# Kernel optimization log

Measured on AMD Instinct MI355X. Metric: run time of the kernel, lower is better.

## Reference

```python
import jax, jax.numpy as jnp
import numpy as np

B, F, Q, E = 256, 128, 4096, 128
TAU = 0.2
P_DROP = 0.5
NUM_SAMPLES = 128  # hardcoded in forward: compute_scores(..., num_samples=128)
NUM_POS = 1
EASY_UB = 0.5
HARD_LB = 0.5


def setup_inputs() -> dict:
    k = jax.random.key(0)
    ks = jax.random.split(k, 8)
    query = jax.random.normal(ks[0], (B, F), jnp.float32)
    key = jax.random.normal(ks[1], (B, F), jnp.float32)
    teacher = jax.random.normal(ks[2], (B, F), jnp.float32)
    negatives = jax.random.normal(ks[3], (F, Q), jnp.float32)
    # random_maskout masks: rand <= p -> zero out
    mask_t = jax.random.uniform(ks[4], (E, B, F)) <= P_DROP
    mask_n = jax.random.uniform(ks[5], (E, F, Q)) <= P_DROP
    # compute_scores sampling mask: rand <= num_samples/Q
    score_mask = jax.random.uniform(ks[6], (E, B, Q)) <= (NUM_SAMPLES / Q)
    # bootstrap over batch dim: for each (e,q) column, sample B row indices with replacement
    idx = jax.random.randint(ks[7], (E, Q, B), 0, B)
    boot = jnp.zeros((E, Q, B), bool).at[
        jnp.arange(E)[:, None, None], jnp.arange(Q)[None, :, None], idx
    ].set(True)
    boot_mask = jnp.transpose(boot, (0, 2, 1))  # (E,B,Q)
    return dict(query=query, key=key, teacher=teacher, negatives=negatives,
                mask_t=mask_t, mask_n=mask_n, score_mask=score_mask, boot_mask=boot_mask)


def _masked_softmax(x, mask, axis):
    # matches torch masked_fill(~mask, -inf) + softmax; masked entries -> 0 prob
    z = jnp.where(mask, x, -jnp.inf)
    m = jnp.max(z, axis=axis, keepdims=True)
    m = jnp.where(jnp.isfinite(m), m, 0.0)  # guard fully-masked slices
    e = jnp.where(mask, jnp.exp(z - m), 0.0)
    return e / jnp.maximum(e.sum(axis=axis, keepdims=True), 1e-30)


def _l2norm(x, axis):
    n = jnp.sqrt(jnp.sum(x * x, axis=axis, keepdims=True))
    return x / jnp.maximum(n, 1e-12)


def reference(query, key, teacher, negatives, mask_t, mask_n, score_mask, boot_mask):
    negatives = jax.lax.stop_gradient(negatives)  # negatives.detach().clone()
    logits_pos = jnp.sum(query * key, axis=1, keepdims=True)      # (B,1)
    logits_neg = query @ negatives                                 # (B,Q)
    logits = jnp.concatenate([logits_pos, logits_neg], axis=1) / TAU
    moco_loss = -jax.nn.log_softmax(logits, axis=1)[:, 0].mean()   # CE with target 0

    # ---- teacher similarities (torch.no_grad) ----
    t = _l2norm(jnp.where(mask_t, 0.0, teacher[None, :, :]), 2)    # (E,B,F)
    n = _l2norm(jnp.where(mask_n, 0.0, negatives[None, :, :]), 1)  # (E,F,Q)
    sim = jax.lax.stop_gradient(jnp.einsum('ebf,efq->ebq', t, n) / TAU)

    # ---- scores: masked softmax over Q, masked mean over E ----
    probs = _masked_softmax(sim, score_mask, axis=2)               # (E,B,Q)
    cnt_e = jnp.maximum(score_mask.sum(axis=0).astype(sim.dtype), 1.0)
    scores = probs.sum(axis=0) / cnt_e                             # (B,Q)

    # ---- uncertainty: masked entropy over batch dim ----
    p = _masked_softmax(sim, boot_mask, axis=1) + 1e-7             # (E,B,Q)
    ent = -(p * jnp.log(p))
    cnt_b = jnp.maximum(boot_mask.sum(axis=1).astype(sim.dtype), 1.0)  # (E,Q)
    uncertainty = (ent.sum(axis=1) / cnt_b).mean(axis=0, keepdims=True)  # (1,Q)

    log_sm_neg = jax.nn.log_softmax(logits[:, 1:], axis=1)         # (B,Q)

    def _pos_loss(pos_mask_row):
        pm = jnp.broadcast_to(pos_mask_row, (B, Q))
        s = jnp.where(pm, scores, -jnp.inf)
        _, idx = jax.lax.top_k(s, NUM_POS)                         # (B,k)
        loss = -jnp.take_along_axis(log_sm_neg, idx, axis=1).mean(axis=1).mean()
        mask = jnp.zeros((B, Q), bool).at[jnp.arange(B)[:, None], idx].set(True)
        return loss, mask

    ub = jnp.quantile(uncertainty, EASY_UB, axis=1)                # (1,)
    easy_loss, easy_mask = _pos_loss(uncertainty <= ub)
    lb = jnp.quantile(uncertainty, HARD_LB, axis=1)
    hard_loss, hard_mask = _pos_loss(uncertainty >= lb)

    return moco_loss, logits, easy_loss, easy_mask, hard_loss, hard_mask
```

## Files before the change

kernel.cpp:

```cpp
#include <hip/hip_runtime.h>
#include <cmath>

typedef unsigned char u8;
typedef unsigned short u16;
typedef unsigned int u32;
typedef __attribute__((ext_vector_type(8))) short s8v;
typedef __attribute__((ext_vector_type(4))) float f32x4;

#define B 256
#define F 128
#define Q 4096
#define E 128
#define QW 128
#define INV_TAU 5.0f
#define CAP 256

#define W_SCORES 0u
#define W_CNT    1048576u
#define W_UNC    2097152u
#define W_CNTB   2101248u
#define W_NLSE   2134016u
#define W_MOCO   2134272u
#define W_EASY   2134528u
#define W_HARD   2134784u
#define W_UB     2135040u
#define W_INVN   2135296u
#define W_AF     2659584u
#define W_PB     4756736u
#define W_PS     8951040u
#define W_PN     13145344u
#define W_ENT    15242496u
#define NZERO    2134016u

#define O_MOCO   0u
#define O_LOGITS 1u
#define O_ELOSS  1048833u
#define O_EMASK  1048834u
#define O_HLOSS  2097410u
#define O_HMASK  2097411u

static __device__ __forceinline__ u16 f2bf(float x) {
    unsigned int u = __builtin_bit_cast(unsigned int, x);
    unsigned int r = (u + 0x7FFFu + ((u >> 16) & 1u)) >> 16;
    return (u16)r;
}

__global__ void k_zero(float4* __restrict__ p) {
    p[(size_t)blockIdx.x * 256 + threadIdx.x] = make_float4(0.f, 0.f, 0.f, 0.f);
}

__global__ void __launch_bounds__(256) k_pack(const u8* __restrict__ boot,
                                              const u8* __restrict__ smask,
                                              const u8* __restrict__ maskn,
                                              u32* __restrict__ pb, u32* __restrict__ ps,
                                              u32* __restrict__ pn) {
    int z = blockIdx.z;
    int Rin = (z == 2) ? F : B;
    if (z == 2 && blockIdx.x >= 2048) return;
    const u8* in = (z == 0) ? boot : (z == 1) ? smask : maskn;
    u32* out = (z == 0) ? pb : (z == 1) ? ps : pn;
    __shared__ u32 lds[64 * 133];
    int t = threadIdx.x;
    int r0 = blockIdx.x * 64;
    int q0 = blockIdx.y * 512;
    int qw0 = q0 >> 5;
    #pragma unroll
    for (int i = 0; i < 8; i++) {
        int w = i * 256 + t;
        int row = w >> 5, c = w & 31;
        uint4 v = *(const uint4*)&in[(size_t)(r0 + row) * Q + q0 + c * 16];
        int base = row * 133 + c * 4;
        lds[base] = v.x; lds[base + 1] = v.y; lds[base + 2] = v.z; lds[base + 3] = v.w;
    }
    __syncthreads();
    int e = r0 / Rin, rr = r0 % Rin;
    #pragma unroll
    for (int k = 0; k < 4; k++) {
        int qw = (t >> 6) + k * 4;
        int r = t & 63;
        u32 w = 0;
        #pragma unroll
        for (int j = 0; j < 8; j++) {
            u32 u = lds[r * 133 + qw * 8 + j];
            w |= ((u & 1u) | ((u >> 7) & 2u) | ((u >> 14) & 4u) | ((u >> 21) & 8u)) << (j * 4);
        }
        out[((size_t)e * QW + qw0 + qw) * Rin + rr + r] = w;
    }
}

__global__ void k_afrag(const float* __restrict__ teacher, const u8* __restrict__ mask_t,
                        u16* __restrict__ af) {
    int eb = blockIdx.x;
    int e  = eb >> 8;
    int b  = eb & (B - 1);
    int f  = threadIdx.x;
    float v = mask_t[(size_t)eb * F + f] ? 0.f : teacher[b * F + f];
    float ss = v * v;
    #pragma unroll
    for (int o = 32; o > 0; o >>= 1) ss += __shfl_down(ss, o);
    __shared__ float s2[2];
    if ((threadIdx.x & 63) == 0) s2[threadIdx.x >> 6] = ss;
    __syncthreads();
    float d = fmaxf(sqrtf(s2[0] + s2[1]), 1e-12f);
    float t = v / d;
    int bg = b >> 4, m = b & 15;
    int kb = f >> 5, quad = (f >> 3) & 3, j = f & 7;
    int lane = quad * 16 + m;
    af[((((size_t)e * 16 + bg) * 4 + kb) * 64 + lane) * 8 + j] = f2bf(t);
}

__global__ void __launch_bounds__(256) k_invn(const float* __restrict__ neg,
                                              const u32* __restrict__ pn,
                                              float* __restrict__ invn) {
    __shared__ u32 lds[32 * 128];
    int e = blockIdx.x, t = threadIdx.x;
    int qblk = blockIdx.y;
    size_t base = ((size_t)e * QW + qblk * 32) * F;
    #pragma unroll
    for (int k = 0; k < 16; k++) lds[t + 256 * k] = pn[base + t + 256 * k];
    __syncthreads();
    int q0 = qblk * 1024 + t * 4;
    int qwl = (t * 4) >> 5;
    int sh = (t * 4) & 31;
    float s0 = 0.f, s1 = 0.f, s2 = 0.f, s3 = 0.f;
    #pragma unroll 4
    for (int f = 0; f < F; f++) {
        float4 v = *(const float4*)&neg[(size_t)f * Q + q0];
        u32 w = lds[qwl * 128 + f] >> sh;
        if (!(w & 1u)) s0 = fmaf(v.x, v.x, s0);
        if (!(w & 2u)) s1 = fmaf(v.y, v.y, s1);
        if (!(w & 4u)) s2 = fmaf(v.z, v.z, s2);
        if (!(w & 8u)) s3 = fmaf(v.w, v.w, s3);
    }
    float4 r;
    r.x = INV_TAU / fmaxf(sqrtf(s0), 1e-12f);
    r.y = INV_TAU / fmaxf(sqrtf(s1), 1e-12f);
    r.z = INV_TAU / fmaxf(sqrtf(s2), 1e-12f);
    r.w = INV_TAU / fmaxf(sqrtf(s3), 1e-12f);
    *(float4*)&invn[(size_t)e * Q + q0] = r;
}

__global__ void __launch_bounds__(256) k_fused(
        const u16* __restrict__ af, const float* __restrict__ neg,
        const u32* __restrict__ pn, const float* __restrict__ invn,
        const u32* __restrict__ pb, const u32* __restrict__ ps,
        float* __restrict__ unc, uint2* __restrict__ ent_buf,
        int* __restrict__ cnt_buf, int e0) {
    __shared__ u16 bfrag[4][4][512];
    __shared__ u32 bw[2][256], sw[2][256];
    __shared__ u32 pnl[2][128];
    __shared__ float invl[64];
    __shared__ float sstat[4][64], cstat[4][64], estat[4][64];
    __shared__ float carr[64];
    __shared__ int sbase[256];

    int qb = blockIdx.x;
    int el = blockIdx.y, e = e0 + el;
    int t = threadIdx.x;
    int q0 = qb * 64;
    int qw0 = qb * 2;

    bw[0][t] = pb[((size_t)e * QW + qw0) * B + t];
    bw[1][t] = pb[((size_t)e * QW + qw0 + 1) * B + t];
    sw[0][t] = ps[((size_t)e * QW + qw0) * B + t];
    sw[1][t] = ps[((size_t)e * QW + qw0 + 1) * B + t];
    if (t < 128) {
        pnl[0][t] = pn[((size_t)e * QW + qw0) * F + t];
        pnl[1][t] = pn[((size_t)e * QW + qw0 + 1) * F + t];
    } else if (t < 192) {
        invl[t - 128] = invn[(size_t)e * Q + q0 + (t - 128)];
    }
    __syncthreads();

    #pragma unroll
    for (int s = 0; s < 4; s++) {
        int slot = t + 256 * s;
        int qg = slot >> 8;
        int r = slot & 255;
        int kb = r >> 6, lane2 = r & 63;
        int ql = qg * 16 + (lane2 & 15);
        int fb = kb * 32 + (lane2 >> 4) * 8;
        float iv = invl[ql];
        const u32* pw = pnl[ql >> 5];
        int sh = ql & 31;
        u16 tmp[8];
        #pragma unroll
        for (int j = 0; j < 8; j++) {
            u32 bit = (pw[fb + j] >> sh) & 1u;
            float v = bit ? 0.f : neg[(size_t)(fb + j) * Q + q0 + ql] * iv;
            tmp[j] = f2bf(v);
        }
        *(s8v*)&bfrag[qg][kb][lane2 * 8] = *(const s8v*)tmp;
    }
    __syncthreads();

    int wave = t >> 6, lane = t & 63;
    int colb = lane & 15, quad = lane >> 4;
    f32x4 acc[4][4];
    #pragma unroll
    for (int bgi = 0; bgi < 4; bgi++) {
        int bg = wave * 4 + bgi;
        s8v a[4];
        #pragma unroll
        for (int kb = 0; kb < 4; kb++)
            a[kb] = *(const s8v*)&af[((((size_t)e * 16 + bg) * 4 + kb) * 64 + lane) * 8];
        #pragma unroll
        for (int qg = 0; qg < 4; qg++) {
            f32x4 c4 = {0.f, 0.f, 0.f, 0.f};
            #pragma unroll
            for (int kb = 0; kb < 4; kb++) {
                s8v bv = *(const s8v*)&bfrag[qg][kb][lane * 8];
                c4 = __builtin_amdgcn_mfma_f32_16x16x32_bf16(a[kb], bv, c4, 0, 0, 0);
            }
            acc[bgi][qg] = c4;
        }
    }

    #pragma unroll
    for (int bgi = 0; bgi < 4; bgi++)
        #pragma unroll
        for (int qg = 0; qg < 4; qg++)
            #pragma unroll
            for (int r = 0; r < 4; r++)
                acc[bgi][qg][r] = __expf(acc[bgi][qg][r]);

    float sloc[4] = {0.f, 0.f, 0.f, 0.f}, cloc[4] = {0.f, 0.f, 0.f, 0.f};
    #pragma unroll
    for (int bgi = 0; bgi < 4; bgi++) {
        int b0 = (wave * 4 + bgi) * 16 + quad * 4;
        uint4 w0 = *(const uint4*)&bw[0][b0];
        uint4 w1 = *(const uint4*)&bw[1][b0];
        u32 W0[4] = {w0.x, w0.y, w0.z, w0.w};
        u32 W1[4] = {w1.x, w1.y, w1.z, w1.w};
        #pragma unroll
        for (int r = 0; r < 4; r++)
            #pragma unroll
            for (int qg = 0; qg < 4; qg++) {
                u32 w = (qg & 2) ? W1[r] : W0[r];
                int bpos = (qg & 1) * 16 + colb;
                if ((w >> bpos) & 1u) {
                    sloc[qg] += acc[bgi][qg][r];
                    cloc[qg] += 1.f;
                }
            }
    }
    #pragma unroll
    for (int qg = 0; qg < 4; qg++) {
        sloc[qg] += __shfl_xor(sloc[qg], 16); sloc[qg] += __shfl_xor(sloc[qg], 32);
        cloc[qg] += __shfl_xor(cloc[qg], 16); cloc[qg] += __shfl_xor(cloc[qg], 32);
    }
    if (quad == 0)
        #pragma unroll
        for (int qg = 0; qg < 4; qg++) {
            sstat[wave][qg * 16 + colb] = sloc[qg];
            cstat[wave][qg * 16 + colb] = cloc[qg];
        }
    __syncthreads();
    float invS[4];
    #pragma unroll
    for (int qg = 0; qg < 4; qg++) {
        int c = qg * 16 + colb;
        float S = sstat[0][c] + sstat[1][c] + sstat[2][c] + sstat[3][c];
        invS[qg] = 1.f / fmaxf(S, 1e-30f);
    }
    if (wave == 0 && quad == 0)
        #pragma unroll
        for (int qg = 0; qg < 4; qg++) {
            int c = qg * 16 + colb;
            carr[c] = cstat[0][c] + cstat[1][c] + cstat[2][c] + cstat[3][c];
        }

    const float P0 = 1e-7f;
    const float C0 = 1.61180954e-6f;
    float eloc[4] = {0.f, 0.f, 0.f, 0.f};
    #pragma unroll
    for (int bgi = 0; bgi < 4; bgi++) {
        int b0 = (wave * 4 + bgi) * 16 + quad * 4;
        uint4 w0 = *(const uint4*)&bw[0][b0];
        uint4 w1 = *(const uint4*)&bw[1][b0];
        u32 W0[4] = {w0.x, w0.y, w0.z, w0.w};
        u32 W1[4] = {w1.x, w1.y, w1.z, w1.w};
        #pragma unroll
        for (int r = 0; r < 4; r++)
            #pragma unroll
            for (int qg = 0; qg < 4; qg++) {
                u32 w = (qg & 2) ? W1[r] : W0[r];
                int bpos = (qg & 1) * 16 + colb;
                if ((w >> bpos) & 1u) {
                    float p = acc[bgi][qg][r] * invS[qg] + P0;
                    eloc[qg] -= p * __logf(p);
                } else {
                    eloc[qg] += C0;
                }
            }
    }
    #pragma unroll
    for (int qg = 0; qg < 4; qg++) {
        eloc[qg] += __shfl_xor(eloc[qg], 16); eloc[qg] += __shfl_xor(eloc[qg], 32);
    }
    if (quad == 0)
        #pragma unroll
        for (int qg = 0; qg < 4; qg++) estat[wave][qg * 16 + colb] = eloc[qg];

    {
        u32 a0 = sw[0][t], a1 = sw[1][t];
        int n = __popc(a0) + __popc(a1);
        int base = 0;
        if (n) base = atomicAdd(&cnt_buf[el * B + t], n);
        sbase[t] = base;
    }
    __syncthreads();

    if (t < 64) {
        float tot = estat[0][t] + estat[1][t] + estat[2][t] + estat[3][t];
        atomicAdd(&unc[q0 + t], tot / fmaxf(carr[t], 1.f));
    }

    u32 cmask = 0x00010001u << colb;
    #pragma unroll
    for (int bgi = 0; bgi < 4; bgi++) {
        int b0 = (wave * 4 + bgi) * 16 + quad * 4;
        uint4 s0 = *(const uint4*)&sw[0][b0];
        uint4 s1 = *(const uint4*)&sw[1][b0];
        u32 S0[4] = {s0.x, s0.y, s0.z, s0.w};
        u32 S1[4] = {s1.x, s1.y, s1.z, s1.w};
        #pragma unroll
        for (int r = 0; r < 4; r++) {
            if (!((S0[r] | S1[r]) & cmask)) continue;
            int bs = sbase[b0 + r];
            int p0 = __popc(S0[r]);
            #pragma unroll
            for (int qg = 0; qg < 4; qg++) {
                int bpos = (qg & 1) * 16 + colb;
                u32 w = (qg & 2) ? S1[r] : S0[r];
                if ((w >> bpos) & 1u) {
                    int rank = __popc(w & ((1u << bpos) - 1u)) + ((qg & 2) ? p0 : 0);
                    int pos = bs + rank;
                    if (pos < CAP) {
                        uint2 en;
                        en.x = (unsigned)(q0 + qg * 16 + colb);
                        en.y = __builtin_bit_cast(unsigned, acc[bgi][qg][r]);
                        ent_buf[((size_t)(el * B + b0 + r)) * CAP + pos] = en;
                    }
                }
            }
        }
    }
}

__global__ void __launch_bounds__(512) k_scores(
        const uint2* __restrict__ ent_buf, const int* __restrict__ cnt_buf,
        float* __restrict__ sacc, float* __restrict__ cacc, int ecnt) {
    __shared__ float srow[Q];
    __shared__ float crow[Q];
    __shared__ int cl[E];
    int b = blockIdx.x, t = threadIdx.x;
    #pragma unroll
    for (int j = 0; j < 8; j++) { srow[t + 512 * j] = 0.f; crow[t + 512 * j] = 0.f; }
    if (t < ecnt) {
        int c = cnt_buf[t * B + b];
        cl[t] = (c > CAP) ? CAP : c;
    }
    __syncthreads();
    int wave = t >> 6, lane = t & 63;
    for (int el = wave; el < ecnt; el += 8) {
        int c = cl[el];
        if (c == 0) continue;
        const uint2* p = ent_buf + (size_t)(el * B + b) * CAP;
        uint2 ev[4]; int ne = 0;
        float s = 0.f;
        for (int i = lane; i < c; i += 64) {
            ev[ne] = p[i];
            s += __builtin_bit_cast(float, ev[ne].y);
            ne++;
        }
        #pragma unroll
        for (int off = 32; off > 0; off >>= 1) s += __shfl_xor(s, off);
        float iS = 1.f / fmaxf(s, 1e-30f);
        for (int k = 0; k < ne; k++) {
            atomicAdd(&srow[ev[k].x], __builtin_bit_cast(float, ev[k].y) * iS);
            atomicAdd(&crow[ev[k].x], 1.f);
        }
    }
    __syncthreads();
    #pragma unroll
    for (int j = 0; j < 8; j++) {
        int q = t + 512 * j;
        sacc[(size_t)b * Q + q] += srow[q];
        cacc[(size_t)b * Q + q] += crow[q];
    }
}

__global__ void k_logits(const float* __restrict__ query, const float* __restrict__ key,
                         const float* __restrict__ neg, float* __restrict__ out) {
    __shared__ float qrow[F];
    __shared__ float red[256];
    int b = blockIdx.x, seg = blockIdx.y, t = threadIdx.x;
    if (t < F) qrow[t] = query[b * F + t];
    __syncthreads();
    int q0 = seg * 1024 + t * 4;
    float4 acc = make_float4(0.f, 0.f, 0.f, 0.f);
    for (int f = 0; f < F; f++) {
        float a = qrow[f];
        float4 v = *(const float4*)&neg[(size_t)f * Q + q0];
        acc.x = fmaf(a, v.x, acc.x);
        acc.y = fmaf(a, v.y, acc.y);
        acc.z = fmaf(a, v.z, acc.z);
        acc.w = fmaf(a, v.w, acc.w);
    }
    float* row = out + O_LOGITS + (size_t)b * (Q + 1);
    row[1 + q0]     = acc.x * INV_TAU;
    row[1 + q0 + 1] = acc.y * INV_TAU;
    row[1 + q0 + 2] = acc.z * INV_TAU;
    row[1 + q0 + 3] = acc.w * INV_TAU;
    if (seg == 0) {
        float pp = (t < F) ? qrow[t] * key[b * F + t] : 0.f;
        red[t] = pp;
        __syncthreads();
        for (int s = 128; s > 0; s >>= 1) { if (t < s) red[t] += red[t + s]; __syncthreads(); }
        if (t == 0) row[0] = red[0] * INV_TAU;
    }
}

__global__ void k_rowstats(const float* __restrict__ out, float* __restrict__ moco_part,
                           float* __restrict__ nlse) {
    __shared__ float red[256];
    int b = blockIdx.x, t = threadIdx.x;
    const float* row = out + O_LOGITS + (size_t)b * (Q + 1);
    float m = -INFINITY, mn = -INFINITY;
    for (int j = 0; j < 17; j++) {
        int i = t + 256 * j;
        if (i < Q + 1) { float zz = row[i]; m = fmaxf(m, zz); if (i >= 1) mn = fmaxf(mn, zz); }
    }
    red[t] = m; __syncthreads();
    for (int s = 128; s > 0; s >>= 1) { if (t < s) red[t] = fmaxf(red[t], red[t + s]); __syncthreads(); }
    float M = red[0]; __syncthreads();
    red[t] = mn; __syncthreads();
    for (int s = 128; s > 0; s >>= 1) { if (t < s) red[t] = fmaxf(red[t], red[t + s]); __syncthreads(); }
    float Mn = red[0]; __syncthreads();
    float s1 = 0.f, s2 = 0.f;
    for (int j = 0; j < 17; j++) {
        int i = t + 256 * j;
        if (i < Q + 1) { float zz = row[i]; s1 += expf(zz - M); if (i >= 1) s2 += expf(zz - Mn); }
    }
    red[t] = s1; __syncthreads();
    for (int s = 128; s > 0; s >>= 1) { if (t < s) red[t] += red[t + s]; __syncthreads(); }
    float S = red[0]; __syncthreads();
    red[t] = s2; __syncthreads();
    for (int s = 128; s > 0; s >>= 1) { if (t < s) red[t] += red[t + s]; __syncthreads(); }
    float Sn = red[0];
    if (t == 0) { moco_part[b] = M + logf(S) - row[0]; nlse[b] = Mn + logf(Sn); }
}

__global__ void k_median(float* __restrict__ unc, float* __restrict__ ubp) {
    __shared__ float sd[4096];
    int t = threadIdx.x;
    #pragma unroll
    for (int j = 0; j < 4; j++) {
        int q = t + 1024 * j;
        float u = unc[q] * (1.f / 128.f);
        unc[q] = u; sd[q] = u;
    }
    __syncthreads();
    for (int k = 2; k <= 4096; k <<= 1) {
        for (int j = k >> 1; j > 0; j >>= 1) {
            #pragma unroll
            for (int base = 0; base < 4; base++) {
                int i = t + 1024 * base;
                int ixj = i ^ j;
                if (ixj > i) {
                    bool up = ((i & k) == 0);
                    float x = sd[i], y = sd[ixj];
                    if ((x > y) == up) { sd[i] = y; sd[ixj] = x; }
                }
            }
            __syncthreads();
        }
    }
    if (t == 0) { float a = sd[2047], b2 = sd[2048]; ubp[0] = a + 0.5f * (b2 - a); }
}

__global__ void k_select(float* __restrict__ out, const float* __restrict__ sacc,
                         const float* __restrict__ cacc,
                         const float* __restrict__ unc, const float* __restrict__ ubp,
                         const float* __restrict__ nlse, float* __restrict__ easy_part,
                         float* __restrict__ hard_part) {
    __shared__ float rv[256];
    __shared__ int ri[256];
    __shared__ int bshare;
    int b = blockIdx.x, mode = blockIdx.y, t = threadIdx.x;
    float ub = ubp[0];
    float bv = -INFINITY; int bidx = Q;
    #pragma unroll
    for (int j = 0; j < 16; j++) {
        int q = t + 256 * j;
        float u = unc[q];
        bool ok = (mode == 0) ? (u <= ub) : (u >= ub);
        if (ok) {
            float v = sacc[(size_t)b * Q + q] / fmaxf(cacc[(size_t)b * Q + q], 1.f);
            if (v > bv || (v == bv && q < bidx)) { bv = v; bidx = q; }
        }
    }
    rv[t] = bv; ri[t] = bidx; __syncthreads();
    for (int s = 128; s > 0; s >>= 1) {
        if (t < s) {
            float v2 = rv[t + s]; int i2 = ri[t + s];
            if (v2 > rv[t] || (v2 == rv[t] && i2 < ri[t])) { rv[t] = v2; ri[t] = i2; }
        }
        __syncthreads();
    }
    if (t == 0) {
        int best = ri[0]; bshare = best;
        float zz = out[O_LOGITS + (size_t)b * (Q + 1) + 1 + best];
        float loss = nlse[b] - zz;
        (mode == 0 ? easy_part : hard_part)[b] = loss;
    }
    __syncthreads();
    int best = bshare;
    float* mrow = out + (mode == 0 ? O_EMASK : O_HMASK) + (size_t)b * Q;
    #pragma unroll
    for (int j = 0; j < 16; j++) { int q = t + 256 * j; mrow[q] = (q == best) ? 1.f : 0.f; }
}

__global__ void k_scalars(const float* __restrict__ moco, const float* __restrict__ easyp,
                          const float* __restrict__ hardp, float* __restrict__ out) {
    __shared__ float red[256];
    int t = threadIdx.x;
    red[t] = moco[t]; __syncthreads();
    for (int s = 128; s > 0; s >>= 1) { if (t < s) red[t] += red[t + s]; __syncthreads(); }
    if (t == 0) out[O_MOCO] = red[0] / 256.f;
    __syncthreads();
    red[t] = easyp[t]; __syncthreads();
    for (int s = 128; s > 0; s >>= 1) { if (t < s) red[t] += red[t + s]; __syncthreads(); }
    if (t == 0) out[O_ELOSS] = red[0] / 256.f;
    __syncthreads();
    red[t] = hardp[t]; __syncthreads();
    for (int s = 128; s > 0; s >>= 1) { if (t < s) red[t] += red[t + s]; __syncthreads(); }
    if (t == 0) out[O_HLOSS] = red[0] / 256.f;
}

extern "C" void kernel_launch(void* const* d_in, const int* in_sizes, int n_in,
                              void* d_out, int out_size, void* d_ws, size_t ws_size,
                              hipStream_t stream) {
    const float* query   = (const float*)d_in[0];
    const float* key     = (const float*)d_in[1];
    const float* teacher = (const float*)d_in[2];
    const float* neg     = (const float*)d_in[3];
    const u8* mask_t     = (const u8*)d_in[4];
    const u8* mask_n     = (const u8*)d_in[5];
    const u8* score_mask = (const u8*)d_in[6];
    const u8* boot_mask  = (const u8*)d_in[7];
    float* out = (float*)d_out;
    float* ws  = (float*)d_ws;

    long ws_floats = (long)(ws_size / 4);
    int Ec = (int)((ws_floats - (long)W_ENT) / (long)(B * CAP * 2));
    if (Ec > E) Ec = E;
    if (Ec < 1) Ec = 1;

    u16* af = (u16*)(ws + W_AF);
    u32* pb = (u32*)(ws + W_PB);
    u32* ps = (u32*)(ws + W_PS);
    u32* pn = (u32*)(ws + W_PN);
    int* cnt_buf = (int*)(ws + W_CNTB);
    uint2* ent_buf = (uint2*)(ws + W_ENT);

    k_zero<<<NZERO / 1024, 256, 0, stream>>>((float4*)(ws + W_SCORES));
    k_pack<<<dim3((E * B) / 64, Q / 512, 3), 256, 0, stream>>>(
        boot_mask, score_mask, mask_n, pb, ps, pn);
    k_afrag<<<E * B, 128, 0, stream>>>(teacher, mask_t, af);
    k_invn<<<dim3(E, 4), 256, 0, stream>>>(neg, pn, ws + W_INVN);
    k_logits<<<dim3(B, 4), 256, 0, stream>>>(query, key, neg, out);
    k_rowstats<<<B, 256, 0, stream>>>(out, ws + W_MOCO, ws + W_NLSE);

    for (int e0 = 0; e0 < E; e0 += Ec) {
        int ecnt = (E - e0 < Ec) ? (E - e0) : Ec;
        if (e0 > 0)
            k_zero<<<32, 256, 0, stream>>>((float4*)(ws + W_CNTB));
        k_fused<<<dim3(Q / 64, ecnt), 256, 0, stream>>>(
            af, neg, pn, ws + W_INVN, pb, ps, ws + W_UNC, ent_buf, cnt_buf, e0);
        k_scores<<<B, 512, 0, stream>>>(ent_buf, cnt_buf,
                                        ws + W_SCORES, ws + W_CNT, ecnt);
    }

    k_median<<<1, 1024, 0, stream>>>(ws + W_UNC, ws + W_UB);
    k_select<<<dim3(B, 2), 256, 0, stream>>>(out, ws + W_SCORES, ws + W_CNT,
                                             ws + W_UNC, ws + W_UB,
                                             ws + W_NLSE, ws + W_EASY, ws + W_HARD);
    k_scalars<<<1, 256, 0, stream>>>(ws + W_MOCO, ws + W_EASY, ws + W_HARD, out);
}
```

Baseline: 1.477 ms.

## Precompute bf16 B-fragments in separate kernel, vectorize afrag, split score accumulation

Adds a k_bprep kernel that builds the masked, normalized bf16 MFMA B-fragments for every (e, q-block) once into a workspace buffer. k_fused then reads these fragments directly from global memory instead of gathering strided neg values and converting them in LDS. k_afrag is rewritten to handle 16 lanes per row with vector loads and shuffle reductions, using far fewer blocks. k_scores is split across two blockIdx.y halves of the E range, each writing its own accumulator copy that k_select sums. The cost is a larger workspace (about 64 MB more for bf), which shrinks the per-chunk Ec and could add chunk iterations if the workspace is limited.

```diff
diff --git a/kernel.cpp b/kernel.cpp
--- a/kernel.cpp
+++ b/kernel.cpp
@@ -16,21 +16,24 @@
 #define CAP 256
 
 #define W_SCORES 0u
-#define W_CNT    1048576u
-#define W_UNC    2097152u
-#define W_CNTB   2101248u
-#define W_NLSE   2134016u
-#define W_MOCO   2134272u
-#define W_EASY   2134528u
-#define W_HARD   2134784u
-#define W_UB     2135040u
-#define W_INVN   2135296u
-#define W_AF     2659584u
-#define W_PB     4756736u
-#define W_PS     8951040u
-#define W_PN     13145344u
-#define W_ENT    15242496u
-#define NZERO    2134016u
+#define W_SC2    1048576u
+#define W_CNT    2097152u
+#define W_CN2    3145728u
+#define W_UNC    4194304u
+#define W_CNTB   4198400u
+#define W_NLSE   4231168u
+#define W_MOCO   4231424u
+#define W_EASY   4231680u
+#define W_HARD   4231936u
+#define W_UB     4232192u
+#define W_INVN   4232448u
+#define W_AF     4756736u
+#define W_PB     6853888u
+#define W_PS     11048192u
+#define W_PN     15242496u
+#define W_BF     17339648u
+#define W_ENT    84448512u
+#define NZERO    4231168u
 
 #define O_MOCO   0u
 #define O_LOGITS 1u
@@ -88,25 +91,38 @@
     }
 }
 
-__global__ void k_afrag(const float* __restrict__ teacher, const u8* __restrict__ mask_t,
-                        u16* __restrict__ af) {
-    int eb = blockIdx.x;
-    int e  = eb >> 8;
-    int b  = eb & (B - 1);
-    int f  = threadIdx.x;
-    float v = mask_t[(size_t)eb * F + f] ? 0.f : teacher[b * F + f];
-    float ss = v * v;
-    #pragma unroll
-    for (int o = 32; o > 0; o >>= 1) ss += __shfl_down(ss, o);
-    __shared__ float s2[2];
-    if ((threadIdx.x & 63) == 0) s2[threadIdx.x >> 6] = ss;
-    __syncthreads();
-    float d = fmaxf(sqrtf(s2[0] + s2[1]), 1e-12f);
-    float t = v / d;
-    int bg = b >> 4, m = b & 15;
-    int kb = f >> 5, quad = (f >> 3) & 3, j = f & 7;
-    int lane = quad * 16 + m;
-    af[((((size_t)e * 16 + bg) * 4 + kb) * 64 + lane) * 8 + j] = f2bf(t);
+__global__ void __launch_bounds__(256) k_afrag(const float* __restrict__ teacher,
+                                               const u8* __restrict__ mask_t,
+                                               u16* __restrict__ af) {
+    int e = blockIdx.x >> 1, h = blockIdx.x & 1;
+    int t = threadIdx.x;
+    int lane16 = t & 15;
+    int f0 = lane16 * 8;
+    #pragma unroll
+    for (int it = 0; it < 8; it++) {
+        int b = h * 128 + it * 16 + (t >> 4);
+        float4 x0 = *(const float4*)&teacher[b * F + f0];
+        float4 x1 = *(const float4*)&teacher[b * F + f0 + 4];
+        const u8* mk = &mask_t[((size_t)e * B + b) * F + f0];
+        float v[8];
+        v[0] = mk[0] ? 0.f : x0.x; v[1] = mk[1] ? 0.f : x0.y;
+        v[2] = mk[2] ? 0.f : x0.z; v[3] = mk[3] ? 0.f : x0.w;
+        v[4] = mk[4] ? 0.f : x1.x; v[5] = mk[5] ? 0.f : x1.y;
+        v[6] = mk[6] ? 0.f : x1.z; v[7] = mk[7] ? 0.f : x1.w;
+        float ss = 0.f;
+        #pragma unroll
+        for (int j = 0; j < 8; j++) ss = fmaf(v[j], v[j], ss);
+        ss += __shfl_xor(ss, 1); ss += __shfl_xor(ss, 2);
+        ss += __shfl_xor(ss, 4); ss += __shfl_xor(ss, 8);
+        float inv = 1.f / fmaxf(sqrtf(ss), 1e-12f);
+        u16 o[8];
+        #pragma unroll
+        for (int j = 0; j < 8; j++) o[j] = f2bf(v[j] * inv);
+        int bg = b >> 4, m = b & 15;
+        int kb = f0 >> 5, quad = (f0 >> 3) & 3;
+        int lane = quad * 16 + m;
+        *(s8v*)&af[((((size_t)e * 16 + bg) * 4 + kb) * 64 + lane) * 8] = *(const s8v*)o;
+    }
 }
 
 __global__ void __launch_bounds__(256) k_invn(const float* __restrict__ neg,
@@ -140,16 +156,51 @@
     *(float4*)&invn[(size_t)e * Q + q0] = r;
 }
 
+__global__ void __launch_bounds__(256) k_bprep(const float* __restrict__ neg,
+                                               const u32* __restrict__ pn,
+                                               const float* __restrict__ invn,
+                                               u16* __restrict__ bf) {
+    __shared__ u16 lf[8192];
+    __shared__ u32 pnl[2][128];
+    __shared__ float invl[64];
+    int e = blockIdx.x, qb = blockIdx.y, t = threadIdx.x;
+    int q0 = qb * 64, qw0 = qb * 2;
+    if (t < 128) pnl[0][t] = pn[((size_t)e * QW + qw0) * F + t];
+    else pnl[1][t - 128] = pn[((size_t)e * QW + qw0 + 1) * F + t - 128];
+    if (t < 16) *(float4*)&invl[t * 4] = *(const float4*)&invn[(size_t)e * Q + q0 + t * 4];
+    __syncthreads();
+    #pragma unroll
+    for (int it = 0; it < 8; it++) {
+        int idx = it * 256 + t;
+        int f = idx >> 4, qq = (idx & 15) * 4;
+        float4 x = *(const float4*)&neg[(size_t)f * Q + q0 + qq];
+        int kb = f >> 5, quad = (f >> 3) & 3, j = f & 7;
+        float xv[4] = {x.x, x.y, x.z, x.w};
+        #pragma unroll
+        for (int c = 0; c < 4; c++) {
+            int ql = qq + c;
+            u32 bit = (pnl[ql >> 5][f] >> (ql & 31)) & 1u;
+            float v = bit ? 0.f : xv[c] * invl[ql];
+            int qg = ql >> 4;
+            int lane = quad * 16 + (ql & 15);
+            lf[(((qg * 4 + kb) * 64) + lane) * 8 + j] = f2bf(v);
+        }
+    }
+    __syncthreads();
+    size_t gb = ((size_t)e * 256 + qb * 4) * 4 * 64 * 8;
+    #pragma unroll
+    for (int it = 0; it < 4; it++) {
+        int s = it * 256 + t;
+        *(s8v*)&bf[gb + (size_t)s * 8] = *(const s8v*)&lf[s * 8];
+    }
+}
+
 __global__ void __launch_bounds__(256) k_fused(
-        const u16* __restrict__ af, const float* __restrict__ neg,
-        const u32* __restrict__ pn, const float* __restrict__ invn,
+        const u16* __restrict__ af, const u16* __restrict__ bf,
         const u32* __restrict__ pb, const u32* __restrict__ ps,
         float* __restrict__ unc, uint2* __restrict__ ent_buf,
         int* __restrict__ cnt_buf, int e0) {
-    __shared__ u16 bfrag[4][4][512];
     __shared__ u32 bw[2][256], sw[2][256];
-    __shared__ u32 pnl[2][128];
-    __shared__ float invl[64];
     __shared__ float sstat[4][64], cstat[4][64], estat[4][64];
     __shared__ float carr[64];
     __shared__ int sbase[256];
@@ -164,38 +215,11 @@
     bw[1][t] = pb[((size_t)e * QW + qw0 + 1) * B + t];
     sw[0][t] = ps[((size_t)e * QW + qw0) * B + t];
     sw[1][t] = ps[((size_t)e * QW + qw0 + 1) * B + t];
-    if (t < 128) {
-        pnl[0][t] = pn[((size_t)e * QW + qw0) * F + t];
-        pnl[1][t] = pn[((size_t)e * QW + qw0 + 1) * F + t];
-    } else if (t < 192) {
-        invl[t - 128] = invn[(size_t)e * Q + q0 + (t - 128)];
-    }
-    __syncthreads();
-
-    #pragma unroll
-    for (int s = 0; s < 4; s++) {
-        int slot = t + 256 * s;
-        int qg = slot >> 8;
-        int r = slot & 255;
-        int kb = r >> 6, lane2 = r & 63;
-        int ql = qg * 16 + (lane2 & 15);
-        int fb = kb * 32 + (lane2 >> 4) * 8;
-        float iv = invl[ql];
-        const u32* pw = pnl[ql >> 5];
-        int sh = ql & 31;
-        u16 tmp[8];
-        #pragma unroll
-        for (int j = 0; j < 8; j++) {
-            u32 bit = (pw[fb + j] >> sh) & 1u;
-            float v = bit ? 0.f : neg[(size_t)(fb + j) * Q + q0 + ql] * iv;
-            tmp[j] = f2bf(v);
-        }
-        *(s8v*)&bfrag[qg][kb][lane2 * 8] = *(const s8v*)tmp;
-    }
     __syncthreads();
 
     int wave = t >> 6, lane = t & 63;
     int colb = lane & 15, quad = lane >> 4;
+    const s8v* bfv = (const s8v*)&bf[((size_t)e * 256 + qb * 4) * 4 * 64 * 8];
     f32x4 acc[4][4];
     #pragma unroll
     for (int bgi = 0; bgi < 4; bgi++) {
@@ -209,7 +233,7 @@
             f32x4 c4 = {0.f, 0.f, 0.f, 0.f};
             #pragma unroll
             for (int kb = 0; kb < 4; kb++) {
-                s8v bv = *(const s8v*)&bfrag[qg][kb][lane * 8];
+                s8v bv = bfv[(qg * 4 + kb) * 64 + lane];
                 c4 = __builtin_amdgcn_mfma_f32_16x16x32_bf16(a[kb], bv, c4, 0, 0, 0);
             }
             acc[bgi][qg] = c4;
@@ -353,24 +377,27 @@
         float* __restrict__ sacc, float* __restrict__ cacc, int ecnt) {
     __shared__ float srow[Q];
     __shared__ float crow[Q];
-    __shared__ int cl[E];
-    int b = blockIdx.x, t = threadIdx.x;
+    __shared__ int cl[64];
+    int b = blockIdx.x, z = blockIdx.y, t = threadIdx.x;
+    int half = (ecnt + 1) >> 1;
+    int el0 = z * half;
+    int nel = ecnt - el0; if (nel > half) nel = half; if (nel < 0) nel = 0;
     #pragma unroll
     for (int j = 0; j < 8; j++) { srow[t + 512 * j] = 0.f; crow[t + 512 * j] = 0.f; }
-    if (t < ecnt) {
-        int c = cnt_buf[t * B + b];
+    if (t < nel) {
+        int c = cnt_buf[(el0 + t) * B + b];
         cl[t] = (c > CAP) ? CAP : c;
     }
     __syncthreads();
     int wave = t >> 6, lane = t & 63;
-    for (int el = wave; el < ecnt; el += 8) {
-        int c = cl[el];
+    for (int i = wave; i < nel; i += 8) {
+        int c = cl[i];
         if (c == 0) continue;
-        const uint2* p = ent_buf + (size_t)(el * B + b) * CAP;
+        const uint2* p = ent_buf + (size_t)((el0 + i) * B + b) * CAP;
         uint2 ev[4]; int ne = 0;
         float s = 0.f;
-        for (int i = lane; i < c; i += 64) {
-            ev[ne] = p[i];
+        for (int k = lane; k < c; k += 64) {
+            ev[ne] = p[k];
             s += __builtin_bit_cast(float, ev[ne].y);
             ne++;
         }
@@ -383,11 +410,13 @@
         }
     }
     __syncthreads();
+    float* sa = sacc + (size_t)z * B * Q;
+    float* ca = cacc + (size_t)z * B * Q;
     #pragma unroll
     for (int j = 0; j < 8; j++) {
         int q = t + 512 * j;
-        sacc[(size_t)b * Q + q] += srow[q];
-        cacc[(size_t)b * Q + q] += crow[q];
+        sa[(size_t)b * Q + q] += srow[q];
+        ca[(size_t)b * Q + q] += crow[q];
     }
 }
 
@@ -497,7 +526,10 @@
         float u = unc[q];
         bool ok = (mode == 0) ? (u <= ub) : (u >= ub);
         if (ok) {
-            float v = sacc[(size_t)b * Q + q] / fmaxf(cacc[(size_t)b * Q + q], 1.f);
+            size_t ix = (size_t)b * Q + q;
+            float s = sacc[ix] + sacc[(size_t)B * Q + ix];
+            float c = cacc[ix] + cacc[(size_t)B * Q + ix];
+            float v = s / fmaxf(c, 1.f);
             if (v > bv || (v == bv && q < bidx)) { bv = v; bidx = q; }
         }
     }
@@ -562,14 +594,16 @@
     u32* pb = (u32*)(ws + W_PB);
     u32* ps = (u32*)(ws + W_PS);
     u32* pn = (u32*)(ws + W_PN);
+    u16* bfr = (u16*)(ws + W_BF);
     int* cnt_buf = (int*)(ws + W_CNTB);
     uint2* ent_buf = (uint2*)(ws + W_ENT);
 
     k_zero<<<NZERO / 1024, 256, 0, stream>>>((float4*)(ws + W_SCORES));
     k_pack<<<dim3((E * B) / 64, Q / 512, 3), 256, 0, stream>>>(
         boot_mask, score_mask, mask_n, pb, ps, pn);
-    k_afrag<<<E * B, 128, 0, stream>>>(teacher, mask_t, af);
+    k_afrag<<<E * 2, 256, 0, stream>>>(teacher, mask_t, af);
     k_invn<<<dim3(E, 4), 256, 0, stream>>>(neg, pn, ws + W_INVN);
+    k_bprep<<<dim3(E, Q / 64), 256, 0, stream>>>(neg, pn, ws + W_INVN, bfr);
     k_logits<<<dim3(B, 4), 256, 0, stream>>>(query, key, neg, out);
     k_rowstats<<<B, 256, 0, stream>>>(out, ws + W_MOCO, ws + W_NLSE);
 
@@ -578,9 +612,9 @@
         if (e0 > 0)
             k_zero<<<32, 256, 0, stream>>>((float4*)(ws + W_CNTB));
         k_fused<<<dim3(Q / 64, ecnt), 256, 0, stream>>>(
-            af, neg, pn, ws + W_INVN, pb, ps, ws + W_UNC, ent_buf, cnt_buf, e0);
-        k_scores<<<B, 512, 0, stream>>>(ent_buf, cnt_buf,
-                                        ws + W_SCORES, ws + W_CNT, ecnt);
+            af, bfr, pb, ps, ws + W_UNC, ent_buf, cnt_buf, e0);
+        k_scores<<<dim3(B, 2), 512, 0, stream>>>(ent_buf, cnt_buf,
+                                                 ws + W_SCORES, ws + W_CNT, ecnt);
     }
 
     k_median<<<1, 1024, 0, stream>>>(ws + W_UNC, ws + W_UB);
```

Result: faster. 1.428 ms (-3.3%).
